# Performance work log

Hardware: AMD Instinct MI355X
Metric: run time of the kernel (lower is better)

Reference implementation:

```python
import jax, jax.numpy as jnp
import numpy as np
from jax import lax

B, C_IN, C_OUT, K, STYLE_DIM, H, W = 8, 512, 512, 3, 512, 64, 64


def setup_inputs() -> dict:
    key = jax.random.key(0)
    k1, k2, k3, k4 = jax.random.split(key, 4)
    return {
        "x": jax.random.normal(k1, (B, C_IN, H, W), dtype=jnp.float32),
        "style": jax.random.normal(k2, (B, STYLE_DIM), dtype=jnp.float32),
        "w": jax.random.normal(k3, (1, C_OUT, C_IN, K, K), dtype=jnp.float32),
        "affine_w": jax.random.normal(k4, (C_IN, STYLE_DIM), dtype=jnp.float32),
        "affine_b": jnp.ones((C_IN,), dtype=jnp.float32),  # bias_init=1
    }


def _per_sample_conv(xi, wi):
    # xi: [C_in, H, W], wi: [C_out, C_in, K, K]; 'same' padding, stride 1
    p = K // 2
    out = lax.conv_general_dilated(
        xi[None], wi, window_strides=(1, 1), padding=[(p, p), (p, p)],
        dimension_numbers=("NCHW", "OIHW", "NCHW"))
    return out[0]


def reference(x, style, w, affine_w, affine_b):
    # Affine (FullyConnected_Layer, linear act, lr_multiplier=1)
    weight_gain_fc = 1.0 / np.sqrt(STYLE_DIM)
    s = style @ (affine_w * weight_gain_fc).T + affine_b  # [B, C_in]

    # Modulate
    weight_gain = 1.0 / np.sqrt(C_IN * K * K)
    weight = w * weight_gain * s[:, None, :, None, None]  # [B, C_out, C_in, K, K]

    # Demodulate
    decoefs = lax.rsqrt(jnp.sum(weight * weight, axis=(2, 3, 4)) + 1e-8)  # [B, C_out]
    weight = weight * decoefs[:, :, None, None, None]

    # Per-sample conv (equivalent to groups=B grouped conv2d)
    out = jax.vmap(_per_sample_conv)(x, weight)  # [B, C_out, H, W]
    return out
```

## Files before the change

### kernel.cpp

```cpp
#include <hip/hip_runtime.h>
#include <hip/hip_bf16.h>


#define CDIM 512
#define HW 64
#define NCHUNK 16
#define XROW 2112

typedef __attribute__((ext_vector_type(8))) short short8;
typedef __attribute__((ext_vector_type(4))) float float4v;

__device__ __forceinline__ short f2bf(float f) {
    unsigned u = __float_as_uint(f);
    unsigned r = (u + 0x7FFFu + ((u >> 16) & 1u)) >> 16;
    return (short)r;
}

__device__ __forceinline__ void async_ld16(const short* g, short* l) {
    __builtin_amdgcn_global_load_lds(
        (const __attribute__((address_space(1))) void*)g,
        (__attribute__((address_space(3))) void*)l, 16, 0, 0);
}

__device__ __forceinline__ void hard_sync() {
    asm volatile("s_waitcnt vmcnt(0) lgkmcnt(0)" ::: "memory");
    __builtin_amdgcn_sched_barrier(0);
    __builtin_amdgcn_s_barrier();
    __builtin_amdgcn_sched_barrier(0);
}


__global__ void k_affine(const float* __restrict__ style, const float* __restrict__ aw,
                         const float* __restrict__ ab, float* __restrict__ s) {
    int gid = blockIdx.x * 4 + (threadIdx.x >> 6);
    int lane = threadIdx.x & 63;
    int b = gid >> 9, ci = gid & 511;
    const float4v* st = (const float4v*)(style + b * CDIM);
    const float4v* wp = (const float4v*)(aw + ci * CDIM);
    float acc = 0.f;
#pragma unroll
    for (int k = 0; k < 2; ++k) {
        float4v a = st[lane * 2 + k], w = wp[lane * 2 + k];
        acc += a[0] * w[0] + a[1] * w[1] + a[2] * w[2] + a[3] * w[3];
    }
#pragma unroll
    for (int off = 32; off; off >>= 1) acc += __shfl_down(acc, off);
    if (lane == 0) s[gid] = acc * 0.04419417382415922f + ab[ci];
}

__global__ void k_ws2(const float* __restrict__ w, float* __restrict__ ws2) {
    int i = blockIdx.x * 256 + threadIdx.x;
    const float* p = w + i * 9;
    float a = 0.f;
#pragma unroll
    for (int t = 0; t < 9; ++t) a += p[t] * p[t];
    ws2[i] = a;
}

__global__ void k_oscale(const float* __restrict__ s, const float* __restrict__ ws2,
                         float* __restrict__ osc) {
    int gid = blockIdx.x * 4 + (threadIdx.x >> 6);
    int lane = threadIdx.x & 63;
    int b = gid >> 9, co = gid & 511;
    const float4v* sp = (const float4v*)(s + b * CDIM);
    const float4v* rp = (const float4v*)(ws2 + co * CDIM);
    float acc = 0.f;
#pragma unroll
    for (int k = 0; k < 2; ++k) {
        float4v a = sp[lane * 2 + k], r = rp[lane * 2 + k];
        acc += a[0] * a[0] * r[0] + a[1] * a[1] * r[1]
             + a[2] * a[2] * r[2] + a[3] * a[3] * r[3];
    }
#pragma unroll
    for (int off = 32; off; off >>= 1) acc += __shfl_down(acc, off);
    const float wg = 0.014731391274719739f;
    const float wg2 = 2.170138888888889e-4f;
    if (lane == 0) osc[gid] = wg * rsqrtf(wg2 * acc + 1e-8f);
}

__global__ void k_wconv(const float* __restrict__ w, short* __restrict__ wgt) {
    int idx = blockIdx.x * 256 + threadIdx.x;
    int j = idx & 7;
    int slotg = idx >> 3;
    int region = slotg / 4608;
    int a16 = slotg - region * 4608;
    int tm = a16 >> 6;
    int t = tm >> 3;
    int mf = tm & 7;
    int sl = a16 & 63;
    int l4 = sl >> 4;
    int l15 = sl & 15;
    int ct = region & 3;
    int c = region >> 2;
    int co = ct * 128 + mf * 16 + l15;
    int ci = c * 32 + l4 * 8 + j;
    wgt[idx] = f2bf(w[(co * CDIM + ci) * 9 + t]);
}

__global__ void k_xs(const float* __restrict__ x, const float* __restrict__ s,
                     short* __restrict__ xs) {
    const int bx = blockIdx.x;
    const int grow = bx & 63;
    const int t = bx >> 6;
    const int c = t & 15;
    const int b = t >> 4;
    const int px = threadIdx.x >> 2;
    const int sl = threadIdx.x & 3;
    const int ci0 = c * 32 + sl * 8;
    const float* xb = x + ((b * CDIM + ci0) * HW + grow) * HW + px;
    const float* sb = s + b * CDIM + ci0;
    short8 pk;
#pragma unroll
    for (int j = 0; j < 8; ++j)
        pk[j] = f2bf(xb[j * (HW * HW)] * sb[j]);
    short* rowp = xs + (size_t)bx * XROW;
    *(short8*)&rowp[(px + 1) * 32 + sl * 8] = pk;
    if (threadIdx.x < 8) {
        int col = (threadIdx.x >> 2) ? 65 : 0;
        int s2 = threadIdx.x & 3;
        short8 z = {};
        *(short8*)&rowp[col * 32 + s2 * 8] = z;
    }
}

__global__ __launch_bounds__(512, 1) void conv_main3(
    const short* __restrict__ xs, const short* __restrict__ zrow,
    const short* __restrict__ wgt, const float* __restrict__ osc,
    float* __restrict__ out) {

    __shared__ __align__(16) short w_lds[2][36864];

    const int tid = threadIdx.x;
    const int lane = tid & 63;
    const int wr = tid >> 6;
    const int l15 = lane & 15;
    const int l4 = lane >> 4;

    const int bx = blockIdx.x;
    const int xcd = bx & 7;
    const int t7 = bx >> 3;
    const int ct = t7 & 3;
    const int ghi = t7 >> 2;
    const int b = xcd;
    const int r0 = ghi * 8;

    const int voff = l15 * 32 + l4 * 8;

    auto stage_w = [&](int c, int bufn) {
        const short* src = wgt + (c * 4 + ct) * 36864;
        short* dstb = &w_lds[bufn][0];
#pragma unroll
        for (int k = 0; k < 9; ++k) {
            int off = (k * 512 + wr * 64) * 8;
            async_ld16(src + off + lane * 8, dstb + off + lane * 8);
        }
    };

    float4v acc[8][4] = {};

#define TAPX(T)                                                                  \
    { const short* pd = ((T) < 3) ? p0 : (((T) < 6) ? p1 : p2);                  \
      const int dwp1 = (T) % 3;                                 \
      short8 bfr[4];                                                             \
      _Pragma("unroll")                                                          \
      for (int nf = 0; nf < 4; ++nf)                                             \
          bfr[nf] = *(const short8*)(pd + voff + (nf * 16 + dwp1) * 32);         \
      _Pragma("unroll")                                                          \
      for (int mf = 0; mf < 8; ++mf) {                                           \
          short8 af = *(const short8*)&wb[(((T) * 8 + mf) * 64 + lane) * 8];     \
          _Pragma("unroll")                                                      \
          for (int nf = 0; nf < 4; ++nf)                                         \
              acc[mf][nf] = __builtin_amdgcn_mfma_f32_16x16x32_bf16(             \
                  af, bfr[nf], acc[mf][nf], 0, 0, 0);                            \
      } }

    stage_w(0, 0);
    hard_sync();

    const int gb = r0 + wr - 1;
#pragma unroll 1
    for (int c = 0; c < NCHUNK; ++c) {
        const int buf = c & 1;
        const short* wb = &w_lds[buf][0];
        const short* xcb = xs + ((size_t)(b * 16 + c) * 64) * XROW;
        const short* p0 = ((unsigned)(gb + 0) < 64u) ? xcb + (size_t)(gb + 0) * XROW : zrow;
        const short* p1 = ((unsigned)(gb + 1) < 64u) ? xcb + (size_t)(gb + 1) * XROW : zrow;
        const short* p2 = ((unsigned)(gb + 2) < 64u) ? xcb + (size_t)(gb + 2) * XROW : zrow;

        TAPX(0)
        stage_w((c + 1 < NCHUNK) ? c + 1 : NCHUNK - 1, buf ^ 1);
        __builtin_amdgcn_s_setprio(1);
        TAPX(1) TAPX(2) TAPX(3) TAPX(4)
        TAPX(5) TAPX(6) TAPX(7) TAPX(8)
        __builtin_amdgcn_s_setprio(0);

        asm volatile("s_waitcnt vmcnt(0)" ::: "memory");
        __builtin_amdgcn_sched_barrier(0);
        __builtin_amdgcn_s_barrier();
        __builtin_amdgcn_sched_barrier(0);
    }
#undef TAPX

    const int row_out = r0 + wr;
#pragma unroll
    for (int mf = 0; mf < 8; ++mf) {
        float4v ov = *(const float4v*)&osc[b * CDIM + ct * 128 + mf * 16 + l4 * 4];
#pragma unroll
        for (int j = 0; j < 4; ++j) {
            int co = ct * 128 + mf * 16 + l4 * 4 + j;
            float* po = out + ((b * CDIM + co) * HW + row_out) * HW;
#pragma unroll
            for (int nf = 0; nf < 4; ++nf)
                po[nf * 16 + l15] = acc[mf][nf][j] * ov[j];
        }
    }
}

__global__ __launch_bounds__(512, 1) void conv_main_fb(
    const float* __restrict__ x, const float* __restrict__ s,
    const short* __restrict__ wgt, const float* __restrict__ osc,
    float* __restrict__ out) {

    __shared__ __align__(16) short w_lds[9 * 8 * 64 * 8];
    __shared__ __align__(16) short x_lds[2][10 * 66 * 32];

    const int tid = threadIdx.x;
    const int lane = tid & 63;
    const int wid = tid >> 6;
    const int l15 = lane & 15;
    const int l4 = lane >> 4;

    const int bx = blockIdx.x;
    const int xcd = bx & 7;
    const int t7 = bx >> 3;
    const int ct = t7 & 3;
    const int ghi = t7 >> 2;
    const int b = xcd;
    const int r0 = ghi * 8;

    const int cig = tid & 3;
    const int col = (tid >> 2) & 63;
    const int rowhalf = tid >> 8;

    for (int i = tid; i < 640; i += 512) {
        int bufi = i >= 320;
        int v = i - bufi * 320;
        int row = v >> 5;
        int w16 = v & 31;
        int colh = (w16 >= 16) ? 65 : 0;
        int q16 = w16 & 15;
        ((unsigned*)x_lds[bufi])[(row * 66 + colh) * 16 + q16] = 0u;
    }

    float rx[40];
    float4v sva, svb;

    auto stage_w = [&](int c) {
        const short* src = wgt + (c * 4 + ct) * 36864;
#pragma unroll
        for (int k = 0; k < 9; ++k) {
            int off = (k * 512 + wid * 64) * 8;
            async_ld16(src + off + lane * 8, w_lds + off);
        }
    };

    auto stage_x_load = [&](int c) {
        const float4v* sp = (const float4v*)&s[b * CDIM + c * 32 + cig * 8];
        sva = sp[0]; svb = sp[1];
#pragma unroll
        for (int i = 0; i < 5; ++i) {
            int row = 2 * i + rowhalf;
            int grow = r0 - 1 + row;
            bool ok = (grow >= 0) && (grow < HW);
            const float* base = x + ((b * CDIM + c * 32 + cig * 8) * HW + (ok ? grow : 0)) * HW + col;
#pragma unroll
            for (int j = 0; j < 8; ++j) {
                float v = base[j * (HW * HW)];
                rx[i * 8 + j] = ok ? v : 0.0f;
            }
        }
    };

    auto stage_x_write = [&](int buf) {
        int lcol = col + 1;
        int q = cig ^ ((lcol >> 1) & 3);
#pragma unroll
        for (int i = 0; i < 5; ++i) {
            int row = 2 * i + rowhalf;
            short8 pk;
#pragma unroll
            for (int j = 0; j < 8; ++j) {
                float sj = (j < 4) ? sva[j] : svb[j - 4];
                pk[j] = f2bf(rx[i * 8 + j] * sj);
            }
            *(short8*)&x_lds[buf][(row * 66 + lcol) * 32 + q * 8] = pk;
        }
    };

    float4v acc[8][4] = {};

    auto compute = [&](int buf) {
        const short* xb = x_lds[buf];
#pragma unroll
        for (int t = 0; t < 9; ++t) {
            int dh = t / 3 - 1;
            int dw = t % 3 - 1;
            int lrow = wid + dh + 1;
            short8 bfr[4];
#pragma unroll
            for (int nf = 0; nf < 4; ++nf) {
                int lcol = 1 + nf * 16 + l15 + dw;
                int xq = l4 ^ ((lcol >> 1) & 3);
                bfr[nf] = *(const short8*)&xb[(lrow * 66 + lcol) * 32 + xq * 8];
            }
#pragma unroll
            for (int mf = 0; mf < 8; ++mf) {
                short8 af = *(const short8*)&w_lds[((t * 8 + mf) * 64 + lane) * 8];
#pragma unroll
                for (int nf = 0; nf < 4; ++nf)
                    acc[mf][nf] = __builtin_amdgcn_mfma_f32_16x16x32_bf16(
                        af, bfr[nf], acc[mf][nf], 0, 0, 0);
            }
        }
    };

    stage_w(0);
    stage_x_load(0);
    stage_x_write(0);
    hard_sync();

    int cur = 0;
#pragma unroll 1
    for (int c = 0; c < NCHUNK; ++c) {
        if (c + 1 < NCHUNK) stage_x_load(c + 1);
        compute(cur);
        if (c + 1 < NCHUNK) {
            hard_sync();
            stage_w(c + 1);
            stage_x_write(cur ^ 1);
            hard_sync();
            cur ^= 1;
        }
    }

    const int row_out = r0 + wid;
#pragma unroll
    for (int mf = 0; mf < 8; ++mf) {
        float4v ov = *(const float4v*)&osc[b * CDIM + ct * 128 + mf * 16 + l4 * 4];
#pragma unroll
        for (int j = 0; j < 4; ++j) {
            int co = ct * 128 + mf * 16 + l4 * 4 + j;
            float* po = out + ((b * CDIM + co) * HW + row_out) * HW;
#pragma unroll
            for (int nf = 0; nf < 4; ++nf)
                po[nf * 16 + l15] = acc[mf][nf][j] * ov[j];
        }
    }
}


extern "C" void kernel_launch(void* const* d_in, const int* in_sizes, int n_in,
                              void* d_out, int out_size, void* d_ws, size_t ws_size,
                              hipStream_t stream) {
    const float* x     = (const float*)d_in[0];
    const float* style = (const float*)d_in[1];
    const float* w     = (const float*)d_in[2];
    const float* aw    = (const float*)d_in[3];
    const float* ab    = (const float*)d_in[4];
    float* out = (float*)d_out;

    char* wsb = (char*)d_ws;
    float* s_buf = (float*)(wsb);
    float* ws2   = (float*)(wsb + 16384);
    float* osc   = (float*)(wsb + 1064960);
    short* wgt   = (short*)(wsb + 1081344);
    short* zrow  = (short*)(wsb + 5799936);
    short* xs    = (short*)(wsb + 5804288);
    const size_t need = 5804288ull + 34603008ull;

    k_affine<<<1024, 256, 0, stream>>>(style, aw, ab, s_buf);
    k_ws2<<<1024, 256, 0, stream>>>(w, ws2);
    k_wconv<<<9216, 256, 0, stream>>>(w, wgt);
    k_oscale<<<1024, 256, 0, stream>>>(s_buf, ws2, osc);

    if (ws_size >= need) {
        hipMemsetAsync(zrow, 0, 4352, stream);
        k_xs<<<8192, 256, 0, stream>>>(x, s_buf, xs);
        conv_main3<<<256, 512, 0, stream>>>(xs, zrow, wgt, osc, out);
    } else {
        conv_main_fb<<<256, 512, 0, stream>>>(x, s_buf, wgt, osc, out);
    }
}
```

Measured before the change: 157.5 us.

## Split output-channel tile to 64 and launch 512 blocks for higher occupancy

Halves the per-block output-channel tile from 128 to 64, so the main conv kernel launches 512 blocks instead of 256 with half the LDS weight buffer and half the accumulators. The weight prepack kernel gets a new layout that matches the smaller tile, and the fallback path keeps the old layout. The aim is to fill all CUs and let several blocks share a CU to hide latency. In exchange, each staged x row is reused by fewer output channels, so activation traffic from global memory doubles.

```diff
diff --git a/kernel.cpp b/kernel.cpp
--- a/kernel.cpp
+++ b/kernel.cpp
@@ -78,7 +78,26 @@
     if (lane == 0) osc[gid] = wg * rsqrtf(wg2 * acc + 1e-8f);
 }
 
-__global__ void k_wconv(const float* __restrict__ w, short* __restrict__ wgt) {
+__global__ void k_wconv8(const float* __restrict__ w, short* __restrict__ wgt) {
+    int idx = blockIdx.x * 256 + threadIdx.x;
+    int j = idx & 7;
+    int slotg = idx >> 3;
+    int region = slotg / 2304;
+    int a16 = slotg - region * 2304;
+    int tm = a16 >> 6;
+    int t = tm >> 2;
+    int mf = tm & 3;
+    int sl = a16 & 63;
+    int l4 = sl >> 4;
+    int l15 = sl & 15;
+    int ct = region & 7;
+    int c = region >> 3;
+    int co = ct * 64 + mf * 16 + l15;
+    int ci = c * 32 + l4 * 8 + j;
+    wgt[idx] = f2bf(w[(co * CDIM + ci) * 9 + t]);
+}
+
+__global__ void k_wconv4(const float* __restrict__ w, short* __restrict__ wgt) {
     int idx = blockIdx.x * 256 + threadIdx.x;
     int j = idx & 7;
     int slotg = idx >> 3;
@@ -123,12 +142,12 @@
     }
 }
 
-__global__ __launch_bounds__(512, 1) void conv_main3(
+__global__ __launch_bounds__(512, 4) void conv_main4(
     const short* __restrict__ xs, const short* __restrict__ zrow,
     const short* __restrict__ wgt, const float* __restrict__ osc,
     float* __restrict__ out) {
 
-    __shared__ __align__(16) short w_lds[2][36864];
+    __shared__ __align__(16) short w_lds[2][18432];
 
     const int tid = threadIdx.x;
     const int lane = tid & 63;
@@ -139,35 +158,36 @@
     const int bx = blockIdx.x;
     const int xcd = bx & 7;
     const int t7 = bx >> 3;
-    const int ct = t7 & 3;
-    const int ghi = t7 >> 2;
+    const int ct = t7 & 7;
+    const int ghi = t7 >> 3;
     const int b = xcd;
     const int r0 = ghi * 8;
 
     const int voff = l15 * 32 + l4 * 8;
 
     auto stage_w = [&](int c, int bufn) {
-        const short* src = wgt + (c * 4 + ct) * 36864;
+        const short* src = wgt + (c * 8 + ct) * 18432;
         short* dstb = &w_lds[bufn][0];
 #pragma unroll
-        for (int k = 0; k < 9; ++k) {
-            int off = (k * 512 + wr * 64) * 8;
-            async_ld16(src + off + lane * 8, dstb + off + lane * 8);
+        for (int k = 0; k < 5; ++k) {
+            int u = tid + 512 * k;
+            if (u >= 2304) u -= 2304;
+            async_ld16(src + u * 8, dstb + u * 8);
         }
     };
 
-    float4v acc[8][4] = {};
+    float4v acc[4][4] = {};
 
 #define TAPX(T)                                                                  \
     { const short* pd = ((T) < 3) ? p0 : (((T) < 6) ? p1 : p2);                  \
-      const int dwp1 = (T) % 3;                                 \
+      const int dwp1 = (T) % 3;                                                  \
       short8 bfr[4];                                                             \
       _Pragma("unroll")                                                          \
       for (int nf = 0; nf < 4; ++nf)                                             \
           bfr[nf] = *(const short8*)(pd + voff + (nf * 16 + dwp1) * 32);         \
       _Pragma("unroll")                                                          \
-      for (int mf = 0; mf < 8; ++mf) {                                           \
-          short8 af = *(const short8*)&wb[(((T) * 8 + mf) * 64 + lane) * 8];     \
+      for (int mf = 0; mf < 4; ++mf) {                                           \
+          short8 af = *(const short8*)&wb[(((T) * 4 + mf) * 64 + lane) * 8];     \
           _Pragma("unroll")                                                      \
           for (int nf = 0; nf < 4; ++nf)                                         \
               acc[mf][nf] = __builtin_amdgcn_mfma_f32_16x16x32_bf16(             \
@@ -203,11 +223,11 @@
 
     const int row_out = r0 + wr;
 #pragma unroll
-    for (int mf = 0; mf < 8; ++mf) {
-        float4v ov = *(const float4v*)&osc[b * CDIM + ct * 128 + mf * 16 + l4 * 4];
+    for (int mf = 0; mf < 4; ++mf) {
+        float4v ov = *(const float4v*)&osc[b * CDIM + ct * 64 + mf * 16 + l4 * 4];
 #pragma unroll
         for (int j = 0; j < 4; ++j) {
-            int co = ct * 128 + mf * 16 + l4 * 4 + j;
+            int co = ct * 64 + mf * 16 + l4 * 4 + j;
             float* po = out + ((b * CDIM + co) * HW + row_out) * HW;
 #pragma unroll
             for (int nf = 0; nf < 4; ++nf)
@@ -380,14 +400,15 @@
 
     k_affine<<<1024, 256, 0, stream>>>(style, aw, ab, s_buf);
     k_ws2<<<1024, 256, 0, stream>>>(w, ws2);
-    k_wconv<<<9216, 256, 0, stream>>>(w, wgt);
     k_oscale<<<1024, 256, 0, stream>>>(s_buf, ws2, osc);
 
     if (ws_size >= need) {
+        k_wconv8<<<9216, 256, 0, stream>>>(w, wgt);
         hipMemsetAsync(zrow, 0, 4352, stream);
         k_xs<<<8192, 256, 0, stream>>>(x, s_buf, xs);
-        conv_main3<<<256, 512, 0, stream>>>(xs, zrow, wgt, osc, out);
+        conv_main4<<<512, 512, 0, stream>>>(xs, zrow, wgt, osc, out);
     } else {
+        k_wconv4<<<9216, 256, 0, stream>>>(w, wgt);
         conv_main_fb<<<256, 512, 0, stream>>>(x, s_buf, wgt, osc, out);
     }
 }
```

Measured after the change: 187.3 us. 19.0% more time.

## Switch main conv to 32x32x16 MFMA with 4 waves covering two rows each

Applied to the files above, without the earlier changes.

The main conv kernel moves from 16x16x32 bf16 MFMA with 8 waves (one output row each) to 32x32x16 MFMA with 4 waves, each computing a 128co x 2-row tile. The weight pre-pack kernel gains a new layout that matches the 32x32 A-fragment, and the old packer is kept for the fallback path. The aim is better register reuse of B fragments and fewer LDS A-fragment reads per FLOP, since the larger MFMA has higher arithmetic density. The cost is halved wave count per CU, which cuts latency hiding, plus a scalar osc load per output element in the epilogue.

```diff
diff --git a/kernel.cpp b/kernel.cpp
--- a/kernel.cpp
+++ b/kernel.cpp
@@ -9,6 +9,7 @@
 
 typedef __attribute__((ext_vector_type(8))) short short8;
 typedef __attribute__((ext_vector_type(4))) float float4v;
+typedef __attribute__((ext_vector_type(16))) float float16v;
 
 __device__ __forceinline__ short f2bf(float f) {
     unsigned u = __float_as_uint(f);
@@ -78,7 +79,25 @@
     if (lane == 0) osc[gid] = wg * rsqrtf(wg2 * acc + 1e-8f);
 }
 
-__global__ void k_wconv(const float* __restrict__ w, short* __restrict__ wgt) {
+__global__ void k_wconv32(const float* __restrict__ w, short* __restrict__ wgt) {
+    int idx = blockIdx.x * 256 + threadIdx.x;
+    int j = idx & 7;
+    int slotg = idx >> 3;
+    int region = slotg / 4608;
+    int a16 = slotg - region * 4608;
+    int sl = a16 & 63;
+    int g = a16 >> 6;
+    int mf = g & 3;
+    int ks = (g >> 2) & 1;
+    int t = g >> 3;
+    int ct = region & 3;
+    int c = region >> 2;
+    int co = ct * 128 + mf * 32 + (sl & 31);
+    int ci = c * 32 + ks * 16 + (sl >> 5) * 8 + j;
+    wgt[idx] = f2bf(w[(co * CDIM + ci) * 9 + t]);
+}
+
+__global__ void k_wconv4(const float* __restrict__ w, short* __restrict__ wgt) {
     int idx = blockIdx.x * 256 + threadIdx.x;
     int j = idx & 7;
     int slotg = idx >> 3;
@@ -123,7 +142,7 @@
     }
 }
 
-__global__ __launch_bounds__(512, 1) void conv_main3(
+__global__ __launch_bounds__(256, 1) void conv_main5(
     const short* __restrict__ xs, const short* __restrict__ zrow,
     const short* __restrict__ wgt, const float* __restrict__ osc,
     float* __restrict__ out) {
@@ -132,66 +151,76 @@
 
     const int tid = threadIdx.x;
     const int lane = tid & 63;
-    const int wr = tid >> 6;
-    const int l15 = lane & 15;
-    const int l4 = lane >> 4;
+    const int wid = tid >> 6;
+    const int l31 = lane & 31;
+    const int lh = lane >> 5;
 
     const int bx = blockIdx.x;
     const int xcd = bx & 7;
     const int t7 = bx >> 3;
     const int ct = t7 & 3;
-    const int ghi = t7 >> 2;
+    const int rt = t7 >> 2;
     const int b = xcd;
-    const int r0 = ghi * 8;
-
-    const int voff = l15 * 32 + l4 * 8;
+    const int wave_r = rt * 8 + wid * 2;
 
     auto stage_w = [&](int c, int bufn) {
         const short* src = wgt + (c * 4 + ct) * 36864;
         short* dstb = &w_lds[bufn][0];
 #pragma unroll
-        for (int k = 0; k < 9; ++k) {
-            int off = (k * 512 + wr * 64) * 8;
-            async_ld16(src + off + lane * 8, dstb + off + lane * 8);
+        for (int k = 0; k < 18; ++k) {
+            int u = tid + 256 * k;
+            async_ld16(src + u * 8, dstb + u * 8);
         }
     };
 
-    float4v acc[8][4] = {};
-
-#define TAPX(T)                                                                  \
-    { const short* pd = ((T) < 3) ? p0 : (((T) < 6) ? p1 : p2);                  \
-      const int dwp1 = (T) % 3;                                 \
-      short8 bfr[4];                                                             \
-      _Pragma("unroll")                                                          \
-      for (int nf = 0; nf < 4; ++nf)                                             \
-          bfr[nf] = *(const short8*)(pd + voff + (nf * 16 + dwp1) * 32);         \
-      _Pragma("unroll")                                                          \
-      for (int mf = 0; mf < 8; ++mf) {                                           \
-          short8 af = *(const short8*)&wb[(((T) * 8 + mf) * 64 + lane) * 8];     \
-          _Pragma("unroll")                                                      \
-          for (int nf = 0; nf < 4; ++nf)                                         \
-              acc[mf][nf] = __builtin_amdgcn_mfma_f32_16x16x32_bf16(             \
-                  af, bfr[nf], acc[mf][nf], 0, 0, 0);                            \
+    float16v acc[4][4] = {};
+
+#define GRP(T, KS)                                                               \
+    { const int dh = (T) / 3 - 1;                                               \
+      const int dw = (T) % 3 - 1;                                               \
+      short8 bfr[4];                                                            \
+      _Pragma("unroll")                                                         \
+      for (int nf = 0; nf < 4; ++nf) {                                          \
+          const short* pd = p[1 + (nf >> 1) + dh];                              \
+          bfr[nf] = *(const short8*)(pd + ((nf & 1) * 32 + l31 + dw + 1) * 32   \
+                                        + (KS) * 16 + lh * 8);                  \
+      }                                                                         \
+      _Pragma("unroll")                                                         \
+      for (int mf = 0; mf < 4; ++mf) {                                          \
+          short8 af = *(const short8*)&wb[((((T) * 2 + (KS)) * 4 + mf) * 64     \
+                                           + lane) * 8];                        \
+          _Pragma("unroll")                                                     \
+          for (int nf = 0; nf < 4; ++nf)                                        \
+              acc[mf][nf] = __builtin_amdgcn_mfma_f32_32x32x16_bf16(            \
+                  af, bfr[nf], acc[mf][nf], 0, 0, 0);                           \
       } }
 
     stage_w(0, 0);
     hard_sync();
 
-    const int gb = r0 + wr - 1;
+    const int gb = wave_r - 1;
 #pragma unroll 1
     for (int c = 0; c < NCHUNK; ++c) {
         const int buf = c & 1;
         const short* wb = &w_lds[buf][0];
         const short* xcb = xs + ((size_t)(b * 16 + c) * 64) * XROW;
-        const short* p0 = ((unsigned)(gb + 0) < 64u) ? xcb + (size_t)(gb + 0) * XROW : zrow;
-        const short* p1 = ((unsigned)(gb + 1) < 64u) ? xcb + (size_t)(gb + 1) * XROW : zrow;
-        const short* p2 = ((unsigned)(gb + 2) < 64u) ? xcb + (size_t)(gb + 2) * XROW : zrow;
-
-        TAPX(0)
+        const short* p[4];
+#pragma unroll
+        for (int i = 0; i < 4; ++i)
+            p[i] = ((unsigned)(gb + i) < 64u) ? xcb + (size_t)(gb + i) * XROW : zrow;
+
+        GRP(0, 0)
         stage_w((c + 1 < NCHUNK) ? c + 1 : NCHUNK - 1, buf ^ 1);
         __builtin_amdgcn_s_setprio(1);
-        TAPX(1) TAPX(2) TAPX(3) TAPX(4)
-        TAPX(5) TAPX(6) TAPX(7) TAPX(8)
+        GRP(0, 1)
+        GRP(1, 0) GRP(1, 1)
+        GRP(2, 0) GRP(2, 1)
+        GRP(3, 0) GRP(3, 1)
+        GRP(4, 0) GRP(4, 1)
+        GRP(5, 0) GRP(5, 1)
+        GRP(6, 0) GRP(6, 1)
+        GRP(7, 0) GRP(7, 1)
+        GRP(8, 0) GRP(8, 1)
         __builtin_amdgcn_s_setprio(0);
 
         asm volatile("s_waitcnt vmcnt(0)" ::: "memory");
@@ -199,19 +228,20 @@
         __builtin_amdgcn_s_barrier();
         __builtin_amdgcn_sched_barrier(0);
     }
-#undef TAPX
-
-    const int row_out = r0 + wr;
-#pragma unroll
-    for (int mf = 0; mf < 8; ++mf) {
-        float4v ov = *(const float4v*)&osc[b * CDIM + ct * 128 + mf * 16 + l4 * 4];
-#pragma unroll
-        for (int j = 0; j < 4; ++j) {
-            int co = ct * 128 + mf * 16 + l4 * 4 + j;
-            float* po = out + ((b * CDIM + co) * HW + row_out) * HW;
-#pragma unroll
-            for (int nf = 0; nf < 4; ++nf)
-                po[nf * 16 + l15] = acc[mf][nf][j] * ov[j];
+#undef GRP
+
+#pragma unroll
+    for (int mf = 0; mf < 4; ++mf) {
+#pragma unroll
+        for (int nf = 0; nf < 4; ++nf) {
+            const int row_out = wave_r + (nf >> 1);
+            const int px = (nf & 1) * 32 + l31;
+#pragma unroll
+            for (int r = 0; r < 16; ++r) {
+                int co = ct * 128 + mf * 32 + (r & 3) + 8 * (r >> 2) + 4 * lh;
+                float oscv = osc[b * CDIM + co];
+                out[((b * CDIM + co) * HW + row_out) * HW + px] = acc[mf][nf][r] * oscv;
+            }
         }
     }
 }
@@ -380,14 +410,15 @@
 
     k_affine<<<1024, 256, 0, stream>>>(style, aw, ab, s_buf);
     k_ws2<<<1024, 256, 0, stream>>>(w, ws2);
-    k_wconv<<<9216, 256, 0, stream>>>(w, wgt);
     k_oscale<<<1024, 256, 0, stream>>>(s_buf, ws2, osc);
 
     if (ws_size >= need) {
+        k_wconv32<<<9216, 256, 0, stream>>>(w, wgt);
         hipMemsetAsync(zrow, 0, 4352, stream);
         k_xs<<<8192, 256, 0, stream>>>(x, s_buf, xs);
-        conv_main3<<<256, 512, 0, stream>>>(xs, zrow, wgt, osc, out);
+        conv_main5<<<256, 256, 0, stream>>>(xs, zrow, wgt, osc, out);
     } else {
+        k_wconv4<<<9216, 256, 0, stream>>>(w, wgt);
         conv_main_fb<<<256, 512, 0, stream>>>(x, s_buf, wgt, osc, out);
     }
 }
```

Measured after the change: 209.9 us. 33.3% more time.
